# Kernel tuning notes

Measured on AMD Instinct MI355X. Metric: run time of the kernel, lower is better.

The kernel has to match this reference:

```python
import jax, jax.numpy as jnp
import numpy as np

B, L1, L2, H = 32, 512, 512, 768


def setup_inputs() -> dict:
    key = jax.random.key(0)
    k1, k2, k3, k4 = jax.random.split(key, 4)
    x = jax.random.normal(k1, (B, L1, H), dtype=jnp.float32)
    y = jax.random.normal(k2, (B, L2, H), dtype=jnp.float32)
    # y_mask: True = padding position to be masked out (torch masked_fill semantics)
    y_mask = jax.random.randint(k3, (B, L2), 0, 2).astype(bool)
    W = jax.random.normal(k4, (H, H), dtype=jnp.float32) * 0.02  # nn.Linear weight [out,in]
    b = jnp.zeros((H,), dtype=jnp.float32)
    return {"x": x, "y": y, "y_mask": y_mask, "W": W, "b": b}


def reference(x, y, y_mask, W, b):
    # Shared linear projection + ReLU on both sequences (nn.Linear: v @ W^T + b)
    x_proj = jax.nn.relu(jnp.einsum('bmh,oh->bmo', x, W) + b)
    y_proj = jax.nn.relu(jnp.einsum('bnh,oh->bno', y, W) + b)
    # Unscaled attention scores [B, L1, L2]
    scores = jnp.einsum('bmh,bnh->bmn', x_proj, y_proj)
    scores = jnp.where(y_mask[:, None, :], -jnp.inf, scores)
    alpha = jax.nn.softmax(scores, axis=-1)
    # Attention-weighted sum over the *original* y (not y_proj)
    matched_seq = jnp.einsum('bmn,bnh->bmh', alpha, y)
    return matched_seq
```

## Files before the change

kernel.cpp:

```cpp
#include <hip/hip_runtime.h>
#include <hip/hip_bf16.h>
#include <math.h>


typedef _Float16 f16x8 __attribute__((ext_vector_type(8)));
typedef float f32x4 __attribute__((ext_vector_type(4)));

__device__ __forceinline__ void gld_lds16(const void* g, void* l) {
  __builtin_amdgcn_global_load_lds(
      (const __attribute__((address_space(1))) unsigned*)g,
      (__attribute__((address_space(3))) unsigned*)l, 16, 0, 0);
}

__global__ __launch_bounds__(256) void cvt_f16_kernel(
    const float* __restrict__ src, _Float16* __restrict__ dst) {
  size_t i = ((size_t)blockIdx.x * 256 + threadIdx.x) * 8;
  float4 a = *(const float4*)&src[i];
  float4 b = *(const float4*)&src[i + 4];
  _Float16 h[8] = {(_Float16)a.x, (_Float16)a.y, (_Float16)a.z, (_Float16)a.w,
                   (_Float16)b.x, (_Float16)b.y, (_Float16)b.z, (_Float16)b.w};
  *(uint4*)&dst[i] = *(uint4*)h;
}

__global__ __launch_bounds__(256) void proj_mfma_kernel(
    const _Float16* __restrict__ A, const _Float16* __restrict__ W,
    const float* __restrict__ bias, _Float16* __restrict__ P) {
  const int K = 768, N = 768;
  __shared__ _Float16 As[128 * 32], Bs[128 * 32];
  int bm = blockIdx.x * 128, bn = blockIdx.y * 128;
  int tid = threadIdx.x, lane = tid & 63, wave = tid >> 6;
  int wm = (wave & 1) * 64, wn = (wave >> 1) * 64;
  int fr = lane & 15, fk = (lane >> 4) * 8;
  int lrow = lane >> 2, lcol = (lane & 3) << 3;

  f32x4 acc[4][4];
#pragma unroll
  for (int i = 0; i < 4; ++i)
#pragma unroll
    for (int j = 0; j < 4; ++j)
#pragma unroll
      for (int e = 0; e < 4; ++e) acc[i][j][e] = 0.f;

  for (int k0 = 0; k0 < K; k0 += 32) {
    __syncthreads();
#pragma unroll
    for (int t = 0; t < 2; ++t) {
      int row = wave * 32 + t * 16;
      gld_lds16(&A[(size_t)(bm + row + lrow) * K + k0 + lcol], &As[row * 32]);
      gld_lds16(&W[(size_t)(bn + row + lrow) * K + k0 + lcol], &Bs[row * 32]);
    }
    __syncthreads();
    f16x8 a[4], bb[4];
#pragma unroll
    for (int i = 0; i < 4; ++i) {
      a[i] = *(const f16x8*)&As[(wm + i * 16 + fr) * 32 + fk];
      bb[i] = *(const f16x8*)&Bs[(wn + i * 16 + fr) * 32 + fk];
    }
#pragma unroll
    for (int i = 0; i < 4; ++i)
#pragma unroll
      for (int j = 0; j < 4; ++j)
        acc[i][j] = __builtin_amdgcn_mfma_f32_16x16x32_f16(a[i], bb[j], acc[i][j], 0, 0, 0);
  }
#pragma unroll
  for (int i = 0; i < 4; ++i)
#pragma unroll
    for (int r = 0; r < 4; ++r) {
      int m = bm + wm + i * 16 + (lane >> 4) * 4 + r;
#pragma unroll
      for (int j = 0; j < 4; ++j) {
        int n = bn + wn + j * 16 + fr;
        P[(size_t)m * N + n] = (_Float16)fmaxf(acc[i][j][r] + bias[n], 0.f);
      }
    }
}

__global__ __launch_bounds__(256) void scores_mfma_kernel(
    const _Float16* __restrict__ Px, const _Float16* __restrict__ Py,
    const int* __restrict__ mask, float* __restrict__ S) {
  const int K = 768, L = 512;
  __shared__ _Float16 As[128 * 32], Bs[128 * 32];
  int b = blockIdx.z;
  size_t pb = (size_t)b * L * K;
  const int* mk = mask + (size_t)b * L;
  float* Sb = S + (size_t)b * L * L;
  int bm = blockIdx.x * 128, bn = blockIdx.y * 128;
  int tid = threadIdx.x, lane = tid & 63, wave = tid >> 6;
  int wm = (wave & 1) * 64, wn = (wave >> 1) * 64;
  int fr = lane & 15, fk = (lane >> 4) * 8;
  int lrow = lane >> 2, lcol = (lane & 3) << 3;

  f32x4 acc[4][4];
#pragma unroll
  for (int i = 0; i < 4; ++i)
#pragma unroll
    for (int j = 0; j < 4; ++j)
#pragma unroll
      for (int e = 0; e < 4; ++e) acc[i][j][e] = 0.f;

  for (int k0 = 0; k0 < K; k0 += 32) {
    __syncthreads();
#pragma unroll
    for (int t = 0; t < 2; ++t) {
      int row = wave * 32 + t * 16;
      gld_lds16(&Px[pb + (size_t)(bm + row + lrow) * K + k0 + lcol], &As[row * 32]);
      gld_lds16(&Py[pb + (size_t)(bn + row + lrow) * K + k0 + lcol], &Bs[row * 32]);
    }
    __syncthreads();
    f16x8 a[4], bb[4];
#pragma unroll
    for (int i = 0; i < 4; ++i) {
      a[i] = *(const f16x8*)&As[(wm + i * 16 + fr) * 32 + fk];
      bb[i] = *(const f16x8*)&Bs[(wn + i * 16 + fr) * 32 + fk];
    }
#pragma unroll
    for (int i = 0; i < 4; ++i)
#pragma unroll
      for (int j = 0; j < 4; ++j)
        acc[i][j] = __builtin_amdgcn_mfma_f32_16x16x32_f16(a[i], bb[j], acc[i][j], 0, 0, 0);
  }
#pragma unroll
  for (int i = 0; i < 4; ++i)
#pragma unroll
    for (int r = 0; r < 4; ++r) {
      int m = bm + wm + i * 16 + (lane >> 4) * 4 + r;
#pragma unroll
      for (int j = 0; j < 4; ++j) {
        int n = bn + wn + j * 16 + fr;
        Sb[(size_t)m * L + n] = mk[n] ? -INFINITY : acc[i][j][r];
      }
    }
}

__global__ __launch_bounds__(256) void softmax_kernel(
    const float* __restrict__ S, _Float16* __restrict__ Alpha) {
  size_t row = blockIdx.x;
  const float* p = S + row * 512;
  _Float16* q = Alpha + row * 512;
  int tid = threadIdx.x, lane = tid & 63, wid = tid >> 6;
  float2 v = *(const float2*)(p + tid * 2);

  float m = fmaxf(v.x, v.y);
#pragma unroll
  for (int off = 32; off > 0; off >>= 1) m = fmaxf(m, __shfl_down(m, off));
  __shared__ float redm[4], reds[4];
  if (lane == 0) redm[wid] = m;
  __syncthreads();
  m = fmaxf(fmaxf(redm[0], redm[1]), fmaxf(redm[2], redm[3]));

  float e0 = __expf(v.x - m);
  float e1 = __expf(v.y - m);
  float s = e0 + e1;
#pragma unroll
  for (int off = 32; off > 0; off >>= 1) s += __shfl_down(s, off);
  if (lane == 0) reds[wid] = s;
  __syncthreads();
  s = reds[0] + reds[1] + reds[2] + reds[3];
  float inv = 1.0f / s;
  q[tid * 2] = (_Float16)(e0 * inv);
  q[tid * 2 + 1] = (_Float16)(e1 * inv);
}

__global__ __launch_bounds__(256) void yT_kernel(const float* __restrict__ Y,
                                                 _Float16* __restrict__ YT) {
  __shared__ _Float16 T[64][65];
  int b = blockIdx.z;
  int n0 = blockIdx.x * 64, h0 = blockIdx.y * 64;
  const float* Yb = Y + (size_t)b * 512 * 768;
  _Float16* Tb = YT + (size_t)b * 768 * 512;
  int tid = threadIdx.x;
  int r = tid >> 4, c = (tid & 15) << 2;
#pragma unroll
  for (int i = 0; i < 4; ++i) {
    int rr = r + i * 16;
    float4 v = *(const float4*)&Yb[(size_t)(n0 + rr) * 768 + h0 + c];
    T[c + 0][rr] = (_Float16)v.x;
    T[c + 1][rr] = (_Float16)v.y;
    T[c + 2][rr] = (_Float16)v.z;
    T[c + 3][rr] = (_Float16)v.w;
  }
  __syncthreads();
  int hr = tid >> 2, nc = (tid & 3) << 4;
  _Float16* dst = &Tb[(size_t)(h0 + hr) * 512 + n0 + nc];
  _Float16 tmp[16];
#pragma unroll
  for (int j = 0; j < 16; ++j) tmp[j] = T[hr][nc + j];
  *(uint4*)&dst[0] = *(uint4*)&tmp[0];
  *(uint4*)&dst[8] = *(uint4*)&tmp[8];
}

__global__ __launch_bounds__(256) void attn_mfma_kernel(
    const _Float16* __restrict__ Alpha, const _Float16* __restrict__ YT,
    float* __restrict__ O) {
  const int L = 512, H = 768;
  __shared__ _Float16 As[128 * 32], Bs[128 * 32];
  int b = blockIdx.z;
  const _Float16* Ab = Alpha + (size_t)b * L * L;
  const _Float16* Yb = YT + (size_t)b * H * L;
  float* Ob = O + (size_t)b * L * H;
  int bm = blockIdx.x * 128, bn = blockIdx.y * 128;
  int tid = threadIdx.x, lane = tid & 63, wave = tid >> 6;
  int wm = (wave & 1) * 64, wn = (wave >> 1) * 64;
  int fr = lane & 15, fk = (lane >> 4) * 8;
  int lrow = lane >> 2, lcol = (lane & 3) << 3;

  f32x4 acc[4][4];
#pragma unroll
  for (int i = 0; i < 4; ++i)
#pragma unroll
    for (int j = 0; j < 4; ++j)
#pragma unroll
      for (int e = 0; e < 4; ++e) acc[i][j][e] = 0.f;

  for (int k0 = 0; k0 < L; k0 += 32) {
    __syncthreads();
#pragma unroll
    for (int t = 0; t < 2; ++t) {
      int row = wave * 32 + t * 16;
      gld_lds16(&Ab[(size_t)(bm + row + lrow) * L + k0 + lcol], &As[row * 32]);
      gld_lds16(&Yb[(size_t)(bn + row + lrow) * L + k0 + lcol], &Bs[row * 32]);
    }
    __syncthreads();
    f16x8 a[4], bb[4];
#pragma unroll
    for (int i = 0; i < 4; ++i) {
      a[i] = *(const f16x8*)&As[(wm + i * 16 + fr) * 32 + fk];
      bb[i] = *(const f16x8*)&Bs[(wn + i * 16 + fr) * 32 + fk];
    }
#pragma unroll
    for (int i = 0; i < 4; ++i)
#pragma unroll
      for (int j = 0; j < 4; ++j)
        acc[i][j] = __builtin_amdgcn_mfma_f32_16x16x32_f16(a[i], bb[j], acc[i][j], 0, 0, 0);
  }
#pragma unroll
  for (int i = 0; i < 4; ++i)
#pragma unroll
    for (int r = 0; r < 4; ++r) {
      int m = bm + wm + i * 16 + (lane >> 4) * 4 + r;
#pragma unroll
      for (int j = 0; j < 4; ++j) {
        int h = bn + wn + j * 16 + fr;
        Ob[(size_t)m * H + h] = acc[i][j][r];
      }
    }
}

extern "C" void kernel_launch(void* const* d_in, const int* in_sizes, int n_in,
                              void* d_out, int out_size, void* d_ws, size_t ws_size,
                              hipStream_t stream) {
  const float* x = (const float*)d_in[0];
  const float* y = (const float*)d_in[1];
  const int* y_mask = (const int*)d_in[2];
  const float* W = (const float*)d_in[3];
  const float* b = (const float*)d_in[4];
  float* out = (float*)d_out;

  const size_t E = (size_t)16384 * 768;
  _Float16* xh = (_Float16*)d_ws;
  _Float16* yh = xh + E;
  _Float16* Px = yh + E;
  _Float16* Py = Px + E;
  float* S = (float*)(Py + E);
  _Float16* Wh = (_Float16*)S;
  _Float16* alpha = xh;
  _Float16* yT = Px;

  dim3 blk(256);
  cvt_f16_kernel<<<dim3(6144), blk, 0, stream>>>(x, xh);
  cvt_f16_kernel<<<dim3(6144), blk, 0, stream>>>(y, yh);
  cvt_f16_kernel<<<dim3(288), blk, 0, stream>>>(W, Wh);
  proj_mfma_kernel<<<dim3(128, 6), blk, 0, stream>>>(xh, Wh, b, Px);
  proj_mfma_kernel<<<dim3(128, 6), blk, 0, stream>>>(yh, Wh, b, Py);
  scores_mfma_kernel<<<dim3(4, 4, 32), blk, 0, stream>>>(Px, Py, y_mask, S);
  yT_kernel<<<dim3(8, 12, 32), blk, 0, stream>>>(y, yT);
  softmax_kernel<<<dim3(32 * 512), blk, 0, stream>>>(S, alpha);
  attn_mfma_kernel<<<dim3(4, 6, 32), blk, 0, stream>>>(alpha, yT, out);
}
```

Measured before the change: 287.3 us.

## Merge conversion and projection launches, switch projection to 32x32x16 MFMA

Folds the three fp32-to-fp16 conversion launches into one kernel and runs both projections as a single launch over the contiguous xh/yh buffers (256 row-blocks writing Px then Py). The projection inner loop moves from 16x16x32 to 32x32x16 MFMA tiles, so fewer LDS fragment reads are needed per MFMA. Workspace buffers are no longer aliased, which uses more scratch memory. The goal is lower launch overhead and better projection throughput.

```diff
diff --git a/kernel.cpp b/kernel.cpp
--- a/kernel.cpp
+++ b/kernel.cpp
@@ -5,6 +5,7 @@
 
 typedef _Float16 f16x8 __attribute__((ext_vector_type(8)));
 typedef float f32x4 __attribute__((ext_vector_type(4)));
+typedef float f32x16 __attribute__((ext_vector_type(16)));
 
 __device__ __forceinline__ void gld_lds16(const void* g, void* l) {
   __builtin_amdgcn_global_load_lds(
@@ -12,9 +13,17 @@
       (__attribute__((address_space(3))) unsigned*)l, 16, 0, 0);
 }
 
-__global__ __launch_bounds__(256) void cvt_f16_kernel(
-    const float* __restrict__ src, _Float16* __restrict__ dst) {
-  size_t i = ((size_t)blockIdx.x * 256 + threadIdx.x) * 8;
+__global__ __launch_bounds__(256) void cvt_all_kernel(
+    const float* __restrict__ x, const float* __restrict__ y,
+    const float* __restrict__ W, _Float16* __restrict__ xh,
+    _Float16* __restrict__ yh, _Float16* __restrict__ Wh) {
+  int blk = blockIdx.x;
+  const float* src;
+  _Float16* dst;
+  if (blk < 6144) { src = x; dst = xh; }
+  else if (blk < 12288) { src = y; dst = yh; blk -= 6144; }
+  else { src = W; dst = Wh; blk -= 12288; }
+  size_t i = ((size_t)blk * 256 + threadIdx.x) * 8;
   float4 a = *(const float4*)&src[i];
   float4 b = *(const float4*)&src[i + 4];
   _Float16 h[8] = {(_Float16)a.x, (_Float16)a.y, (_Float16)a.z, (_Float16)a.w,
@@ -30,16 +39,16 @@
   int bm = blockIdx.x * 128, bn = blockIdx.y * 128;
   int tid = threadIdx.x, lane = tid & 63, wave = tid >> 6;
   int wm = (wave & 1) * 64, wn = (wave >> 1) * 64;
-  int fr = lane & 15, fk = (lane >> 4) * 8;
+  int r32 = lane & 31, g = lane >> 5;
   int lrow = lane >> 2, lcol = (lane & 3) << 3;
 
-  f32x4 acc[4][4];
-#pragma unroll
-  for (int i = 0; i < 4; ++i)
-#pragma unroll
-    for (int j = 0; j < 4; ++j)
-#pragma unroll
-      for (int e = 0; e < 4; ++e) acc[i][j][e] = 0.f;
+  f32x16 acc[2][2];
+#pragma unroll
+  for (int i = 0; i < 2; ++i)
+#pragma unroll
+    for (int j = 0; j < 2; ++j)
+#pragma unroll
+      for (int e = 0; e < 16; ++e) acc[i][j][e] = 0.f;
 
   for (int k0 = 0; k0 < K; k0 += 32) {
     __syncthreads();
@@ -50,27 +59,33 @@
       gld_lds16(&W[(size_t)(bn + row + lrow) * K + k0 + lcol], &Bs[row * 32]);
     }
     __syncthreads();
-    f16x8 a[4], bb[4];
-#pragma unroll
-    for (int i = 0; i < 4; ++i) {
-      a[i] = *(const f16x8*)&As[(wm + i * 16 + fr) * 32 + fk];
-      bb[i] = *(const f16x8*)&Bs[(wn + i * 16 + fr) * 32 + fk];
-    }
-#pragma unroll
-    for (int i = 0; i < 4; ++i)
-#pragma unroll
-      for (int j = 0; j < 4; ++j)
-        acc[i][j] = __builtin_amdgcn_mfma_f32_16x16x32_f16(a[i], bb[j], acc[i][j], 0, 0, 0);
-  }
-#pragma unroll
-  for (int i = 0; i < 4; ++i)
-#pragma unroll
-    for (int r = 0; r < 4; ++r) {
-      int m = bm + wm + i * 16 + (lane >> 4) * 4 + r;
-#pragma unroll
-      for (int j = 0; j < 4; ++j) {
-        int n = bn + wn + j * 16 + fr;
-        P[(size_t)m * N + n] = (_Float16)fmaxf(acc[i][j][r] + bias[n], 0.f);
+    f16x8 a[2][2], bb[2][2];
+#pragma unroll
+    for (int i = 0; i < 2; ++i)
+#pragma unroll
+      for (int h = 0; h < 2; ++h) {
+        a[i][h] = *(const f16x8*)&As[(wm + 32 * i + r32) * 32 + h * 16 + g * 8];
+        bb[i][h] = *(const f16x8*)&Bs[(wn + 32 * i + r32) * 32 + h * 16 + g * 8];
+      }
+#pragma unroll
+    for (int i = 0; i < 2; ++i)
+#pragma unroll
+      for (int j = 0; j < 2; ++j)
+#pragma unroll
+        for (int h = 0; h < 2; ++h)
+          acc[i][j] = __builtin_amdgcn_mfma_f32_32x32x16_f16(a[i][h], bb[j][h], acc[i][j], 0, 0, 0);
+  }
+#pragma unroll
+  for (int i = 0; i < 2; ++i)
+#pragma unroll
+    for (int j = 0; j < 2; ++j) {
+      int n = bn + wn + 32 * j + r32;
+      float bv = bias[n];
+#pragma unroll
+      for (int e = 0; e < 16; ++e) {
+        int row = (e & 3) + 8 * (e >> 2) + 4 * g;
+        int m = bm + wm + 32 * i + row;
+        P[(size_t)m * N + n] = (_Float16)fmaxf(acc[i][j][e] + bv, 0.f);
       }
     }
 }
@@ -262,16 +277,13 @@
   _Float16* Px = yh + E;
   _Float16* Py = Px + E;
   float* S = (float*)(Py + E);
-  _Float16* Wh = (_Float16*)S;
-  _Float16* alpha = xh;
-  _Float16* yT = Px;
+  _Float16* Wh = (_Float16*)(S + (size_t)32 * 512 * 512);
+  _Float16* yT = Wh + (size_t)768 * 768;
+  _Float16* alpha = yT + E;
 
   dim3 blk(256);
-  cvt_f16_kernel<<<dim3(6144), blk, 0, stream>>>(x, xh);
-  cvt_f16_kernel<<<dim3(6144), blk, 0, stream>>>(y, yh);
-  cvt_f16_kernel<<<dim3(288), blk, 0, stream>>>(W, Wh);
-  proj_mfma_kernel<<<dim3(128, 6), blk, 0, stream>>>(xh, Wh, b, Px);
-  proj_mfma_kernel<<<dim3(128, 6), blk, 0, stream>>>(yh, Wh, b, Py);
+  cvt_all_kernel<<<dim3(12576), blk, 0, stream>>>(x, y, W, xh, yh, Wh);
+  proj_mfma_kernel<<<dim3(256, 6), blk, 0, stream>>>(xh, Wh, b, Px);
   scores_mfma_kernel<<<dim3(4, 4, 32), blk, 0, stream>>>(Px, Py, y_mask, S);
   yT_kernel<<<dim3(8, 12, 32), blk, 0, stream>>>(y, yT);
   softmax_kernel<<<dim3(32 * 512), blk, 0, stream>>>(S, alpha);
```

Result: no change. 288.6 us (+0.4%).
